# Optimization experiments

Measured on AMD Instinct MI355X. Metric: run time of the kernel, lower is better.

Reference implementation:

```python
import jax, jax.numpy as jnp
import numpy as np

N, E, IN, H1, H2, A, B, MAXB = 57344, 458752, 128, 256, 64, 11, 16, 4096
GD = H1  # g_dim = hidden1


def _lin(k, i, o):
    return jax.random.normal(k, (i, o), jnp.float32) / np.sqrt(i).astype(np.float32)


def setup_inputs():
    key = jax.random.key(0)
    ks = jax.random.split(key, 24)
    x = jax.random.normal(ks[0], (N, IN), jnp.float32)
    x = x.at[:, 0].set(1.0)  # every node is a host (x[:,0]==1)
    ei = jax.random.randint(ks[1], (2, E), 0, N, dtype=jnp.int32)
    sizes = [4096] * 12 + [2048] * 4  # sums to N
    batches = jnp.asarray(np.concatenate([[0], np.cumsum(sizes)]), jnp.int32)
    inp = {
        'x': x, 'ei': ei, 'batches': batches, 'max_batch': MAXB,
        'conv1_w': _lin(ks[2], IN, H1), 'conv1_b': jnp.zeros((H1,), jnp.float32),
        'conv2_w': _lin(ks[3], H1, H2), 'conv2_b': jnp.zeros((H2,), jnp.float32),
        # SimpleSelfAttention g0: in=IN, h=H1, g=GD
        'g0_aw': _lin(ks[4], IN, H1), 'g0_ab': jnp.zeros((H1,), jnp.float32),
        'g0_fw': _lin(ks[5], IN, H1), 'g0_fb': jnp.zeros((H1,), jnp.float32),
        'g0_gw': _lin(ks[6], H1 + GD, GD), 'g0_gb': jnp.zeros((GD,), jnp.float32),
        # g1: in=H1, h=H1, g=GD
        'g1_aw': _lin(ks[7], H1, H1), 'g1_ab': jnp.zeros((H1,), jnp.float32),
        'g1_fw': _lin(ks[8], H1, H1), 'g1_fb': jnp.zeros((H1,), jnp.float32),
        'g1_gw': _lin(ks[9], H1 + GD, GD), 'g1_gb': jnp.zeros((GD,), jnp.float32),
        # g2: in=H2, h=H2, g=GD
        'g2_aw': _lin(ks[10], H2, H2), 'g2_ab': jnp.zeros((H2,), jnp.float32),
        'g2_fw': _lin(ks[11], H2, H2), 'g2_fb': jnp.zeros((H2,), jnp.float32),
        'g2_gw': _lin(ks[12], H2 + GD, GD), 'g2_gb': jnp.zeros((GD,), jnp.float32),
        # out MLP head
        'o1_w': _lin(ks[13], H2 + GD, H1), 'o1_b': jnp.zeros((H1,), jnp.float32),
        'o2_w': _lin(ks[14], H1, A), 'o2_b': jnp.zeros((A,), jnp.float32),
    }
    return inp


def reference(x, ei, batches, max_batch,
              conv1_w, conv1_b, conv2_w, conv2_b,
              g0_aw, g0_ab, g0_fw, g0_fb, g0_gw, g0_gb,
              g1_aw, g1_ab, g1_fw, g1_fb, g1_gw, g1_gb,
              g2_aw, g2_ab, g2_fw, g2_fb, g2_gw, g2_gb,
              o1_w, o1_b, o2_w, o2_b):
    n = x.shape[0]
    nb = batches.shape[0] - 1
    idx = jnp.arange(n, dtype=jnp.int32)
    # all nodes are hosts; CSR -> (batch_id, position) for vectorized pad_and_pack
    batch_id = jnp.searchsorted(batches, idx, side='right').astype(jnp.int32) - 1
    pos = idx - batches[batch_id]
    mask = jnp.zeros((nb, max_batch, 1), x.dtype).at[batch_id, pos].set(1.0)

    def pack(h):  # [n, d] -> [nb, max_batch, d] with zero padding
        return jnp.zeros((nb, max_batch, h.shape[-1]), h.dtype).at[batch_id, pos].set(h)

    src_sl = jnp.concatenate([ei[0], idx])  # add self loops
    dst_sl = jnp.concatenate([ei[1], idx])

    def gcn(h, W, b):  # GCNConv: D^{-1/2}(A+I)D^{-1/2} h W + b (deg from target col)
        deg = jax.ops.segment_sum(jnp.ones_like(dst_sl, h.dtype), dst_sl, num_segments=n)
        dis = jnp.where(deg > 0, jax.lax.rsqrt(jnp.maximum(deg, 1.0)), 0.0)
        norm = dis[src_sl] * dis[dst_sl]
        hw = h @ W
        return jax.ops.segment_sum(hw[src_sl] * norm[:, None], dst_sl, num_segments=n) + b

    def attn(v, g, aw, ab, fw, fb, gw, gb):  # SimpleSelfAttention
        att = jax.nn.softmax(v @ aw + ab, axis=-1) * mask
        feat = v @ fw + fb
        o = jnp.sum(att * feat, axis=1)  # [nb, h]
        return g + (jnp.concatenate([o, g], axis=-1) @ gw + gb)

    g = attn(pack(x), jnp.zeros((nb, GD), x.dtype), g0_aw, g0_ab, g0_fw, g0_fb, g0_gw, g0_gb)
    h = jax.nn.relu(gcn(x, conv1_w, conv1_b))
    g = attn(pack(h), g, g1_aw, g1_ab, g1_fw, g1_fb, g1_gw, g1_gb)
    h = jax.nn.relu(gcn(h, conv2_w, conv2_b))
    g = attn(pack(h), g, g2_aw, g2_ab, g2_fw, g2_fb, g2_gw, g2_gb)

    host_z = jnp.concatenate([h, g[batch_id]], axis=1)  # repeat_interleave via gather
    actions = jax.nn.relu(host_z @ o1_w + o1_b) @ o2_w + o2_b  # [n, A]
    out = pack(actions)  # [nb, max_batch, A]
    out = jnp.where(mask > 0, out, -jnp.inf)
    return out.reshape(nb, max_batch * A)  # Categorical logits
```

## Files before the change

### kernel.cpp

```cpp
#include <hip/hip_runtime.h>
#include <math.h>

#define N_NODES 57344
#define N_EDGES 458752
#define DIM_IN 128
#define DIM_H1 256
#define DIM_H2 64
#define DIM_A 11
#define NB 16
#define MAXB 4096
#define OUT_PER_B (MAXB*DIM_A)
#define OUT_SZ (NB*OUT_PER_B)
#define NEG_FILL (-1.0e30f)

typedef unsigned short u16;
typedef unsigned int u32;
typedef __bf16 bf16x8 __attribute__((ext_vector_type(8)));
typedef float f32x4 __attribute__((ext_vector_type(4)));

__device__ __forceinline__ float bflo(u32 u){ union{u32 i; float f;} x; x.i = u<<16; return x.f; }
__device__ __forceinline__ float bfhi(u32 u){ union{u32 i; float f;} x; x.i = u & 0xFFFF0000u; return x.f; }
__device__ __forceinline__ u32 f2bf(float f){ union{float f; u32 i;} x; x.f=f; return (x.i + 0x7FFFu + ((x.i>>16)&1u)) >> 16; }

__device__ __forceinline__ float wave_max(float v){
  #pragma unroll
  for (int off=32; off; off>>=1) v = fmaxf(v, __shfl_xor(v, off));
  return v;
}
__device__ __forceinline__ float wave_sum(float v){
  #pragma unroll
  for (int off=32; off; off>>=1) v += __shfl_xor(v, off);
  return v;
}

__global__ __launch_bounds__(256) void k_init(int* cnt, int* bid, const int* __restrict__ batches,
                                              float* oacc, float* out){
  int i = blockIdx.x*256 + threadIdx.x;
  if (i < N_NODES){
    cnt[i] = 0;
    int lo=0, hi=NB-1;
    while (lo<hi){ int mid=(lo+hi+1)>>1; if (batches[mid]<=i) lo=mid; else hi=mid-1; }
    bid[i]=lo;
  }
  if (i < 3*NB*256) oacc[i] = 0.0f;
  if (i < OUT_SZ) out[i] = NEG_FILL;
}

__global__ __launch_bounds__(256) void k_deg(const int* __restrict__ ei, int* cnt){
  int e = blockIdx.x*256 + threadIdx.x;
  if (e < N_EDGES) atomicAdd(&cnt[ei[N_EDGES + e]], 1);
}

__global__ __launch_bounds__(256) void k_scanA(const int* __restrict__ cnt, int* bsum){
  __shared__ int s[256];
  int t=threadIdx.x; int i=blockIdx.x*256+t;
  s[t]=cnt[i]; __syncthreads();
  for (int off=128; off; off>>=1){ if (t<off) s[t]+=s[t+off]; __syncthreads(); }
  if (t==0) bsum[blockIdx.x]=s[0];
}
__global__ __launch_bounds__(256) void k_scanB(const int* __restrict__ bsum, int* boff){
  __shared__ int s[256];
  int t=threadIdx.x;
  int v = (t < N_NODES/256) ? bsum[t] : 0;
  s[t]=v; __syncthreads();
  for (int o=1;o<256;o<<=1){
    int a = (t>=o) ? s[t-o] : 0;
    __syncthreads();
    s[t] += a;
    __syncthreads();
  }
  if (t < N_NODES/256) boff[t] = s[t] - v;
}
__global__ __launch_bounds__(256) void k_scanC(const int* __restrict__ cnt, const int* __restrict__ boff,
                                               int* rowstart, int* cursor, float* dis){
  __shared__ int s[256];
  int t=threadIdx.x; int i=blockIdx.x*256+t;
  int v=cnt[i]; s[t]=v; __syncthreads();
  for (int off=1; off<256; off<<=1){
    int add = (t>=off)? s[t-off] : 0;
    __syncthreads();
    s[t]+=add;
    __syncthreads();
  }
  int rs = boff[blockIdx.x] + s[t] - v;
  rowstart[i]=rs; cursor[i]=rs;
  dis[i] = rsqrtf(1.0f + (float)v);
}
__global__ __launch_bounds__(256) void k_place(const int* __restrict__ ei, int* cursor, int* csr_src){
  int e = blockIdx.x*256 + threadIdx.x;
  if (e < N_EDGES){
    int s = ei[e], d = ei[N_EDGES+e];
    int slot = atomicAdd(&cursor[d], 1);
    csr_src[slot] = s;
  }
}

__global__ __launch_bounds__(256) void k_cvtx(const float* __restrict__ x, u16* __restrict__ xb){
  int i = blockIdx.x*256 + threadIdx.x;
  float4 v = *(const float4*)(x + (size_t)i*4);
  u32 lo = f2bf(v.x) | (f2bf(v.y)<<16);
  u32 hi = f2bf(v.z) | (f2bf(v.w)<<16);
  *(uint2*)(xb + (size_t)i*4) = make_uint2(lo, hi);
}

__global__ __launch_bounds__(256) void k_prep(
    const float* __restrict__ conv1_w, const float* __restrict__ g0_aw, const float* __restrict__ g0_fw,
    const float* __restrict__ g1_aw, const float* __restrict__ g1_fw, const float* __restrict__ conv2_w,
    const float* __restrict__ g2_aw, const float* __restrict__ g2_fw, const float* __restrict__ o1_w,
    const float* __restrict__ g0_ab, const float* __restrict__ g0_fb,
    const float* __restrict__ g1_ab, const float* __restrict__ g1_fb,
    const float* __restrict__ g2_ab, const float* __restrict__ g2_fb,
    u16* conv1T, u16* Wt0, u16* Wt1, u16* conv2T, u16* Wt2, u16* o1T,
    float* cb0, float* cb1, float* cb2){
  int i = blockIdx.x*256 + threadIdx.x;
  if (i < 32768){ int k=i>>8, n=i&255; conv1T[n*128+k]=(u16)f2bf(conv1_w[i]); return; } i-=32768;
  if (i < 32768){ int k=i>>8, n=i&255; Wt0[n*128+k]=(u16)f2bf(g0_aw[i]); return; } i-=32768;
  if (i < 32768){ int k=i>>8, n=i&255; Wt0[(256+n)*128+k]=(u16)f2bf(g0_fw[i]); return; } i-=32768;
  if (i < 65536){ int k=i>>8, n=i&255; Wt1[n*256+k]=(u16)f2bf(g1_aw[i]); return; } i-=65536;
  if (i < 65536){ int k=i>>8, n=i&255; Wt1[(256+n)*256+k]=(u16)f2bf(g1_fw[i]); return; } i-=65536;
  if (i < 16384){ int k=i>>6, n=i&63;  conv2T[n*256+k]=(u16)f2bf(conv2_w[i]); return; } i-=16384;
  if (i < 4096) { int k=i>>6, n=i&63;  Wt2[n*64+k]=(u16)f2bf(g2_aw[i]); return; } i-=4096;
  if (i < 4096) { int k=i>>6, n=i&63;  Wt2[(64+n)*64+k]=(u16)f2bf(g2_fw[i]); return; } i-=4096;
  if (i < 16384){ int k=i>>8, n=i&255; o1T[n*64+k]=(u16)f2bf(o1_w[i]); return; } i-=16384;
  if (i < 256){ cb0[i]=g0_ab[i]; return; } i-=256;
  if (i < 256){ cb0[256+i]=g0_fb[i]; return; } i-=256;
  if (i < 256){ cb1[i]=g1_ab[i]; return; } i-=256;
  if (i < 256){ cb1[256+i]=g1_fb[i]; return; } i-=256;
  if (i < 64) { cb2[i]=g2_ab[i]; return; } i-=64;
  if (i < 64) { cb2[64+i]=g2_fb[i]; return; }
}

__global__ __launch_bounds__(256) void k_agg1b(const u16* __restrict__ xb, const float* __restrict__ dis,
        const int* __restrict__ rowstart, const int* __restrict__ cnt, const int* __restrict__ csr_src,
        u16* __restrict__ agg){
  int d = (blockIdx.x*256 + threadIdx.x) >> 6;
  int lane = threadIdx.x & 63;
  float dd = dis[d];
  u32 u = *(const u32*)(xb + (size_t)d*DIM_IN + lane*2);
  float ax = bflo(u)*dd*dd, ay = bfhi(u)*dd*dd;
  int base = rowstart[d], c = cnt[d];
  int j = 0;
  for (; j+4 <= c; j += 4){
    int s0=csr_src[base+j+0], s1=csr_src[base+j+1], s2=csr_src[base+j+2], s3=csr_src[base+j+3];
    u32 u0=*(const u32*)(xb+(size_t)s0*DIM_IN+lane*2);
    u32 u1=*(const u32*)(xb+(size_t)s1*DIM_IN+lane*2);
    u32 u2=*(const u32*)(xb+(size_t)s2*DIM_IN+lane*2);
    u32 u3=*(const u32*)(xb+(size_t)s3*DIM_IN+lane*2);
    float n0=dis[s0]*dd, n1=dis[s1]*dd, n2=dis[s2]*dd, n3=dis[s3]*dd;
    ax=fmaf(bflo(u0),n0,ax); ay=fmaf(bfhi(u0),n0,ay);
    ax=fmaf(bflo(u1),n1,ax); ay=fmaf(bfhi(u1),n1,ay);
    ax=fmaf(bflo(u2),n2,ax); ay=fmaf(bfhi(u2),n2,ay);
    ax=fmaf(bflo(u3),n3,ax); ay=fmaf(bfhi(u3),n3,ay);
  }
  for (; j<c; ++j){
    int s = csr_src[base+j];
    float nrm = dis[s]*dd;
    u32 us = *(const u32*)(xb + (size_t)s*DIM_IN + lane*2);
    ax = fmaf(bflo(us), nrm, ax);
    ay = fmaf(bfhi(us), nrm, ay);
  }
  *(u32*)(agg + (size_t)d*DIM_IN + lane*2) = f2bf(ax) | (f2bf(ay)<<16);
}

__global__ __launch_bounds__(256) void k_agg2b(const u16* __restrict__ hw, const float* __restrict__ dis,
        const int* __restrict__ rowstart, const int* __restrict__ cnt, const int* __restrict__ csr_src,
        const float* __restrict__ b2, u16* __restrict__ h2){
  int d = (blockIdx.x*256 + threadIdx.x) >> 6;
  int lane = threadIdx.x & 63;
  float dd = dis[d];
  float acc = bflo((u32)hw[(size_t)d*DIM_H2 + lane]) * dd*dd;
  int base = rowstart[d], c = cnt[d];
  int j = 0;
  for (; j+4 <= c; j += 4){
    int s0=csr_src[base+j+0], s1=csr_src[base+j+1], s2=csr_src[base+j+2], s3=csr_src[base+j+3];
    u16 v0=hw[(size_t)s0*DIM_H2+lane], v1=hw[(size_t)s1*DIM_H2+lane];
    u16 v2=hw[(size_t)s2*DIM_H2+lane], v3=hw[(size_t)s3*DIM_H2+lane];
    float n0=dis[s0]*dd, n1=dis[s1]*dd, n2=dis[s2]*dd, n3=dis[s3]*dd;
    acc=fmaf(bflo((u32)v0),n0,acc); acc=fmaf(bflo((u32)v1),n1,acc);
    acc=fmaf(bflo((u32)v2),n2,acc); acc=fmaf(bflo((u32)v3),n3,acc);
  }
  for (; j<c; ++j){
    int s = csr_src[base+j];
    acc = fmaf(bflo((u32)hw[(size_t)s*DIM_H2 + lane]), dis[s]*dd, acc);
  }
  h2[(size_t)d*DIM_H2 + lane] = (u16)f2bf(fmaxf(acc + b2[lane], 0.0f));
}

__global__ __launch_bounds__(256) void k_mm(const u16* __restrict__ A, const u16* __restrict__ Wt,
        const float* __restrict__ bias, const float* __restrict__ rowbias, const int* __restrict__ bid,
        u16* __restrict__ C, int K, int Ncol, int flags){
  __shared__ u16 As[128][40];
  __shared__ u16 Bs[64][40];
  const int t = threadIdx.x;
  const int row0 = blockIdx.x*128, col0 = blockIdx.y*64;
  const int lane = t & 63, w = t >> 6;
  const int lr = lane & 15, q = lane >> 4;
  f32x4 acc[2][4];
  #pragma unroll
  for (int r=0;r<2;++r){
    #pragma unroll
    for (int c=0;c<4;++c){ f32x4 z = {}; acc[r][c] = z; }
  }
  for (int k0=0; k0<K; k0+=32){
    #pragma unroll
    for (int i=0;i<2;++i){
      int ch = t + i*256;
      int r = ch>>2, ko = (ch&3)*8;
      *(uint4*)(&As[r][ko]) = *(const uint4*)(A + (size_t)(row0+r)*K + k0 + ko);
    }
    {
      int r = t>>2, ko = (t&3)*8;
      *(uint4*)(&Bs[r][ko]) = *(const uint4*)(Wt + (size_t)(col0+r)*K + k0 + ko);
    }
    __syncthreads();
    bf16x8 af0 = *(const bf16x8*)(&As[w*32 + lr][q*8]);
    bf16x8 af1 = *(const bf16x8*)(&As[w*32 + 16 + lr][q*8]);
    #pragma unroll
    for (int c=0;c<4;++c){
      bf16x8 bfr = *(const bf16x8*)(&Bs[c*16 + lr][q*8]);
      acc[0][c] = __builtin_amdgcn_mfma_f32_16x16x32_bf16(af0, bfr, acc[0][c], 0,0,0);
      acc[1][c] = __builtin_amdgcn_mfma_f32_16x16x32_bf16(af1, bfr, acc[1][c], 0,0,0);
    }
    __syncthreads();
  }
  float bcol[4];
  #pragma unroll
  for (int c=0;c<4;++c){
    int col = col0 + c*16 + lr;
    float bv = 0.f;
    if (flags & 4) bv += bias[col];
    if (flags & 2) bv += rowbias[(size_t)bid[row0]*Ncol + col];
    bcol[c] = bv;
  }
  #pragma unroll
  for (int r=0;r<2;++r){
    #pragma unroll
    for (int c=0;c<4;++c){
      int col = col0 + c*16 + lr;
      #pragma unroll
      for (int i=0;i<4;++i){
        int row = row0 + w*32 + r*16 + q*4 + i;
        float v = acc[r][c][i] + bcol[c];
        if (flags & 1) v = fmaxf(v, 0.f);
        C[(size_t)row*Ncol + col] = (u16)f2bf(v);
      }
    }
  }
}

template<int DIN>
__global__ __launch_bounds__(256,2) void k_attn4(const u16* __restrict__ V, const u16* __restrict__ Wt,
        const float* __restrict__ cb, const int* __restrict__ bid, float* __restrict__ o){
  constexpr int KS  = DIN/32;
  constexpr int NJ  = 8*KS;
  constexpr int AST = DIN + 8;
  __shared__ u16 As[128*AST];
  __shared__ u16 Bs[2][64][40];
  const int t = threadIdx.x;
  const int node0 = blockIdx.x*128;
  const int lane = t & 63, w = t >> 6;
  const int lr = lane & 15, q = lane >> 4;
  #pragma unroll
  for (int i = 0; i < 128*DIN/(8*256); ++i){
    int ch = t + i*256;
    int r = ch / (DIN/8), co = (ch % (DIN/8))*8;
    *(uint4*)(&As[r*AST + co]) = *(const uint4*)(V + (size_t)(node0+r)*DIN + co);
  }
  auto stageB = [&](int j, int buf){
    int chunk = j / KS, k0 = j % KS;
    int r = t>>2, ko = (t&3)*8;
    *(uint4*)(&Bs[buf][r][ko]) = *(const uint4*)(Wt + (size_t)(chunk*64 + r)*DIN + k0*32 + ko);
  };
  f32x4 sacc[4][2][4];
  #pragma unroll
  for (int cc=0;cc<4;++cc)
    #pragma unroll
    for (int rf=0;rf<2;++rf)
      #pragma unroll
      for (int cf=0;cf<4;++cf){ f32x4 z = {}; sacc[cc][rf][cf] = z; }
  stageB(0, 0);
  __syncthreads();
  #pragma unroll
  for (int j=0; j<4*KS; ++j){
    if (j+1 < NJ) stageB(j+1, (j+1)&1);
    const int k0 = j % KS, chunk = j / KS, buf = j & 1;
    bf16x8 a0 = *(const bf16x8*)(&As[(w*32 + lr)*AST + k0*32 + q*8]);
    bf16x8 a1 = *(const bf16x8*)(&As[(w*32 + 16 + lr)*AST + k0*32 + q*8]);
    #pragma unroll
    for (int cf=0;cf<4;++cf){
      bf16x8 b = *(const bf16x8*)(&Bs[buf][cf*16 + lr][q*8]);
      sacc[chunk][0][cf] = __builtin_amdgcn_mfma_f32_16x16x32_bf16(a0, b, sacc[chunk][0][cf], 0,0,0);
      sacc[chunk][1][cf] = __builtin_amdgcn_mfma_f32_16x16x32_bf16(a1, b, sacc[chunk][1][cf], 0,0,0);
    }
    __syncthreads();
  }
  #pragma unroll
  for (int cc=0;cc<4;++cc)
    #pragma unroll
    for (int cf=0;cf<4;++cf){
      float bv = cb[cc*64 + cf*16 + lr];
      #pragma unroll
      for (int rf=0;rf<2;++rf)
        #pragma unroll
        for (int i=0;i<4;++i) sacc[cc][rf][cf][i] += bv;
    }
  float m[2][4], iz[2][4];
  #pragma unroll
  for (int rf=0;rf<2;++rf){
    #pragma unroll
    for (int i=0;i<4;++i){
      float mx = -1e30f;
      #pragma unroll
      for (int cc=0;cc<4;++cc)
        #pragma unroll
        for (int cf=0;cf<4;++cf) mx = fmaxf(mx, sacc[cc][rf][cf][i]);
      #pragma unroll
      for (int off=1; off<16; off<<=1) mx = fmaxf(mx, __shfl_xor(mx, off));
      float zz = 0.f;
      #pragma unroll
      for (int cc=0;cc<4;++cc)
        #pragma unroll
        for (int cf=0;cf<4;++cf) zz += __expf(sacc[cc][rf][cf][i] - mx);
      #pragma unroll
      for (int off=1; off<16; off<<=1) zz += __shfl_xor(zz, off);
      m[rf][i] = mx; iz[rf][i] = 1.0f/zz;
    }
  }
  const int bb = bid[node0];
  f32x4 facc[2][4];
  #pragma unroll
  for (int rf=0;rf<2;++rf)
    #pragma unroll
    for (int cf=0;cf<4;++cf){ f32x4 z = {}; facc[rf][cf] = z; }
  #pragma unroll
  for (int j=4*KS; j<NJ; ++j){
    if (j+1 < NJ) stageB(j+1, (j+1)&1);
    const int k0 = j % KS, chunk = j / KS, buf = j & 1;
    bf16x8 a0 = *(const bf16x8*)(&As[(w*32 + lr)*AST + k0*32 + q*8]);
    bf16x8 a1 = *(const bf16x8*)(&As[(w*32 + 16 + lr)*AST + k0*32 + q*8]);
    #pragma unroll
    for (int cf=0;cf<4;++cf){
      bf16x8 b = *(const bf16x8*)(&Bs[buf][cf*16 + lr][q*8]);
      facc[0][cf] = __builtin_amdgcn_mfma_f32_16x16x32_bf16(a0, b, facc[0][cf], 0,0,0);
      facc[1][cf] = __builtin_amdgcn_mfma_f32_16x16x32_bf16(a1, b, facc[1][cf], 0,0,0);
    }
    if (k0 == KS-1){
      const int sc = chunk - 4;
      #pragma unroll
      for (int cf=0;cf<4;++cf){
        float fb = cb[chunk*64 + cf*16 + lr];
        float cs = 0.f;
        #pragma unroll
        for (int rf=0;rf<2;++rf)
          #pragma unroll
          for (int i=0;i<4;++i){
            float p = __expf(sacc[sc][rf][cf][i] - m[rf][i]) * iz[rf][i];
            cs = fmaf(p, facc[rf][cf][i] + fb, cs);
          }
        cs += __shfl_xor(cs, 16);
        cs += __shfl_xor(cs, 32);
        if (q == 0) atomicAdd(&o[bb*256 + sc*64 + cf*16 + lr], cs);
      }
      #pragma unroll
      for (int rf=0;rf<2;++rf)
        #pragma unroll
        for (int cf=0;cf<4;++cf){ f32x4 z = {}; facc[rf][cf] = z; }
    }
    __syncthreads();
  }
}

template<int DIN, int H>
__global__ __launch_bounds__(256) void k_attnf(const u16* __restrict__ V, const u16* __restrict__ Wt,
        const float* __restrict__ cb, const int* __restrict__ bid, float* __restrict__ o){
  constexpr int CF  = H/64;
  constexpr int KS  = DIN/32;
  constexpr int AST = DIN + 8;
  constexpr int SST = H + 4;
  __shared__ u16 As[32*AST];
  __shared__ u16 Ssh[32*SST];
  __shared__ u16 Fsh[32*SST];
  __shared__ float mZ[2][32];
  const int t = threadIdx.x;
  const int node0 = blockIdx.x*32;
  const int lane = t & 63, w = t >> 6;
  const int lr = lane & 15, q = lane >> 4;
  #pragma unroll
  for (int i = 0; i < (32*DIN/8)/256; ++i){
    int ch = t + i*256;
    int r = ch / (DIN/8), co = (ch % (DIN/8))*8;
    *(uint4*)(&As[r*AST + co]) = *(const uint4*)(V + (size_t)(node0+r)*DIN + co);
  }
  __syncthreads();
  #pragma unroll
  for (int ph = 0; ph < 2; ++ph){
    f32x4 acc[2][CF];
    #pragma unroll
    for (int r=0;r<2;++r){
      #pragma unroll
      for (int c=0;c<CF;++c){ f32x4 z = {}; acc[r][c] = z; }
    }
    #pragma unroll
    for (int k=0;k<KS;++k){
      bf16x8 a0 = *(const bf16x8*)(&As[lr*AST + k*32 + q*8]);
      bf16x8 a1 = *(const bf16x8*)(&As[(16+lr)*AST + k*32 + q*8]);
      #pragma unroll
      for (int c=0;c<CF;++c){
        int col = ph*H + w*(16*CF) + c*16 + lr;
        bf16x8 b = *(const bf16x8*)(Wt + (size_t)col*DIN + k*32 + q*8);
        acc[0][c] = __builtin_amdgcn_mfma_f32_16x16x32_bf16(a0, b, acc[0][c], 0,0,0);
        acc[1][c] = __builtin_amdgcn_mfma_f32_16x16x32_bf16(a1, b, acc[1][c], 0,0,0);
      }
    }
    u16* dst = ph ? Fsh : Ssh;
    #pragma unroll
    for (int c=0;c<CF;++c){
      int colL = w*(16*CF) + c*16 + lr;
      float bias = cb[ph*H + colL];
      #pragma unroll
      for (int rf=0; rf<2; ++rf){
        #pragma unroll
        for (int i=0;i<4;++i){
          int row = rf*16 + q*4 + i;
          dst[row*SST + colL] = (u16)f2bf(acc[rf][c][i] + bias);
        }
      }
    }
    if (ph==0){
      __syncthreads();
      #pragma unroll
      for (int nn=0; nn<8; ++nn){
        int n = w*8 + nn;
        constexpr int VPL = H/64;
        float vals[VPL]; float mx = -1e30f;
        if constexpr (VPL == 4){
          uint2 uv = *(const uint2*)(&Ssh[n*SST + lane*4]);
          vals[0]=bflo(uv.x); vals[1]=bfhi(uv.x); vals[2]=bflo(uv.y); vals[3]=bfhi(uv.y);
          mx = fmaxf(fmaxf(vals[0],vals[1]), fmaxf(vals[2],vals[3]));
        } else {
          vals[0] = bflo((u32)Ssh[n*SST + lane]);
          mx = vals[0];
        }
        mx = wave_max(mx);
        float z = 0.f;
        #pragma unroll
        for (int i=0;i<VPL;++i) z += __expf(vals[i]-mx);
        z = wave_sum(z);
        if (lane==0){ mZ[0][n]=mx; mZ[1][n]=1.0f/z; }
      }
    }
  }
  __syncthreads();
  const int col = t % H;
  constexpr int NPER = 32*H/256;
  const int n0 = (t / H) * NPER;
  float acc2 = 0.f;
  #pragma unroll 8
  for (int n=n0; n<n0+NPER; ++n){
    float s = bflo((u32)Ssh[n*SST + col]);
    float f = bflo((u32)Fsh[n*SST + col]);
    acc2 = fmaf(__expf(s - mZ[0][n]) * mZ[1][n], f, acc2);
  }
  atomicAdd(&o[bid[node0]*H + col], acc2);
}

template<int H, bool HASG>
__global__ __launch_bounds__(256) void k_gup2(const float* __restrict__ o, const float* __restrict__ gprev,
        const float* __restrict__ gw, const float* __restrict__ gb, float* __restrict__ gout){
  constexpr int KT = H + (HASG ? 256 : 0);
  constexpr int KPS = KT/8;
  __shared__ float vsh[KT];
  __shared__ float red[8][33];
  const int b = blockIdx.x;
  const int c = threadIdx.x & 31;
  const int s = threadIdx.x >> 5;
  const int col = blockIdx.y*32 + c;
  for (int k=threadIdx.x; k<KT; k+=256)
    vsh[k] = (k < H) ? o[b*H + k] : gprev[b*256 + (k - H)];
  __syncthreads();
  float acc = 0.f;
  const float* wp = gw + (size_t)(s*KPS)*256 + col;
  #pragma unroll 8
  for (int i=0;i<KPS;++i)
    acc = fmaf(vsh[s*KPS+i], wp[(size_t)i*256], acc);
  red[s][c] = acc;
  __syncthreads();
  if (s==0){
    float sum = 0.f;
    #pragma unroll
    for (int j=0;j<8;++j) sum += red[j][c];
    float gp = HASG ? gprev[b*256+col] : 0.f;
    gout[b*256+col] = gp + sum + gb[col];
  }
}

__global__ __launch_bounds__(256) void k_hb2(const float* __restrict__ g2, const float* __restrict__ o1w,
                                             const float* __restrict__ o1b, float* __restrict__ hb){
  __shared__ float vsh[256];
  __shared__ float red[8][33];
  const int b = blockIdx.x;
  const int c = threadIdx.x & 31;
  const int s = threadIdx.x >> 5;
  const int col = blockIdx.y*32 + c;
  vsh[threadIdx.x] = g2[b*256 + threadIdx.x];
  __syncthreads();
  float acc = 0.f;
  const float* wp = o1w + (size_t)(64 + s*32)*256 + col;
  #pragma unroll 8
  for (int i=0;i<32;++i)
    acc = fmaf(vsh[s*32+i], wp[(size_t)i*256], acc);
  red[s][c] = acc;
  __syncthreads();
  if (s==0){
    float sum = 0.f;
    #pragma unroll
    for (int j=0;j<8;++j) sum += red[j][c];
    hb[b*256+col] = sum + o1b[col];
  }
}

__global__ __launch_bounds__(256) void k_head2(const u16* __restrict__ z, const float* __restrict__ w,
        const float* __restrict__ bvec, const int* __restrict__ bid, const int* __restrict__ batches,
        float* __restrict__ out){
  __shared__ float zs[16][257];
  int t = threadIdx.x;
  int g0 = blockIdx.x*16;
  #pragma unroll
  for (int i=0;i<2;++i){
    int ch = t + i*256;
    int v = ch>>5, ko=(ch&31)*8;
    uint4 qv = *(const uint4*)(z + (size_t)(g0+v)*256 + ko);
    zs[v][ko+0]=bflo(qv.x); zs[v][ko+1]=bfhi(qv.x);
    zs[v][ko+2]=bflo(qv.y); zs[v][ko+3]=bfhi(qv.y);
    zs[v][ko+4]=bflo(qv.z); zs[v][ko+5]=bfhi(qv.z);
    zs[v][ko+6]=bflo(qv.w); zs[v][ko+7]=bfhi(qv.w);
  }
  __syncthreads();
  int v = t >> 4, c = t & 15;
  if (c < DIM_A){
    float acc = bvec[c];
    for (int k=0;k<256;++k) acc = fmaf(zs[v][k], w[k*DIM_A + c], acc);
    int node = g0 + v;
    int bb = bid[node];
    out[(size_t)bb*OUT_PER_B + (size_t)(node - batches[bb])*DIM_A + c] = acc;
  }
}

extern "C" void kernel_launch(void* const* d_in, const int* in_sizes, int n_in,
                              void* d_out, int out_size, void* d_ws, size_t ws_size,
                              hipStream_t stream){
  const float* x       = (const float*)d_in[0];
  const int*   ei      = (const int*)d_in[1];
  const int*   batches = (const int*)d_in[2];
  const float* conv1_w = (const float*)d_in[4];
  const float* conv1_b = (const float*)d_in[5];
  const float* conv2_w = (const float*)d_in[6];
  const float* conv2_b = (const float*)d_in[7];
  const float* g0_aw = (const float*)d_in[8];  const float* g0_ab = (const float*)d_in[9];
  const float* g0_fw = (const float*)d_in[10]; const float* g0_fb = (const float*)d_in[11];
  const float* g0_gw = (const float*)d_in[12]; const float* g0_gb = (const float*)d_in[13];
  const float* g1_aw = (const float*)d_in[14]; const float* g1_ab = (const float*)d_in[15];
  const float* g1_fw = (const float*)d_in[16]; const float* g1_fb = (const float*)d_in[17];
  const float* g1_gw = (const float*)d_in[18]; const float* g1_gb = (const float*)d_in[19];
  const float* g2_aw = (const float*)d_in[20]; const float* g2_ab = (const float*)d_in[21];
  const float* g2_fw = (const float*)d_in[22]; const float* g2_fb = (const float*)d_in[23];
  const float* g2_gw = (const float*)d_in[24]; const float* g2_gb = (const float*)d_in[25];
  const float* o1_w  = (const float*)d_in[26]; const float* o1_b  = (const float*)d_in[27];
  const float* o2_w  = (const float*)d_in[28]; const float* o2_b  = (const float*)d_in[29];
  float* out = (float*)d_out;

  char* W = (char*)d_ws;
  size_t off = 0;
  auto alloc = [&](size_t bytes)->void*{
    off = (off + 255) & ~(size_t)255;
    void* p = W + off; off += bytes; return p;
  };
  float* dis      = (float*)alloc(N_NODES*4);
  int*   cnt      = (int*)  alloc(N_NODES*4);
  int*   bid      = (int*)  alloc(N_NODES*4);
  int*   rowstart = (int*)  alloc(N_NODES*4);
  int*   cursor   = (int*)  alloc(N_NODES*4);
  int*   csr_src  = (int*)  alloc(N_EDGES*4);
  int*   bsum     = (int*)  alloc(256*4);
  int*   boff     = (int*)  alloc(256*4);
  float* o0       = (float*)alloc(NB*256*4);
  float* o1a      = (float*)alloc(NB*256*4);
  float* o2a      = (float*)alloc(NB*256*4);
  float* gv0      = (float*)alloc(NB*256*4);
  float* gv1      = (float*)alloc(NB*256*4);
  float* gv2      = (float*)alloc(NB*256*4);
  float* hb       = (float*)alloc(NB*256*4);
  float* cb0      = (float*)alloc(512*4);
  float* cb1      = (float*)alloc(512*4);
  float* cb2      = (float*)alloc(128*4);
  u16* conv1T = (u16*)alloc(32768*2);
  u16* Wt0    = (u16*)alloc(65536*2);
  u16* Wt1    = (u16*)alloc(131072*2);
  u16* conv2T = (u16*)alloc(16384*2);
  u16* Wt2    = (u16*)alloc(8192*2);
  u16* o1T    = (u16*)alloc(16384*2);
  u16* h1b    = (u16*)alloc((size_t)N_NODES*DIM_H1*2);
  u16* X      = (u16*)alloc((size_t)N_NODES*DIM_IN*2);
  u16* agg1b  = (u16*)alloc((size_t)N_NODES*DIM_IN*2);
  u16* xb    = X;
  u16* hw2b  = X;
  u16* h2b   = X + (size_t)N_NODES*DIM_H2;
  u16* z     = h1b;

  k_init <<<OUT_SZ/256, 256, 0, stream>>>(cnt, bid, batches, o0, out);
  k_deg  <<<N_EDGES/256, 256, 0, stream>>>(ei, cnt);
  k_scanA<<<N_NODES/256, 256, 0, stream>>>(cnt, bsum);
  k_scanB<<<1, 256, 0, stream>>>(bsum, boff);
  k_scanC<<<N_NODES/256, 256, 0, stream>>>(cnt, boff, rowstart, cursor, dis);
  k_place<<<N_EDGES/256, 256, 0, stream>>>(ei, cursor, csr_src);

  k_cvtx <<<N_NODES*DIM_IN/4/256, 256, 0, stream>>>(x, xb);
  k_prep <<<(270336+1152+255)/256, 256, 0, stream>>>(conv1_w, g0_aw, g0_fw, g1_aw, g1_fw, conv2_w,
            g2_aw, g2_fw, o1_w, g0_ab, g0_fb, g1_ab, g1_fb, g2_ab, g2_fb,
            conv1T, Wt0, Wt1, conv2T, Wt2, o1T, cb0, cb1, cb2);

  k_agg1b<<<N_NODES/4, 256, 0, stream>>>(xb, dis, rowstart, cnt, csr_src, agg1b);
  k_mm   <<<dim3(N_NODES/128, 4), 256, 0, stream>>>(agg1b, conv1T, conv1_b, nullptr, nullptr,
                                                    h1b, DIM_IN, DIM_H1, 4|1);
  k_attn4<128><<<N_NODES/128, 256, 0, stream>>>(xb, Wt0, cb0, bid, o0);
  k_gup2<256,false><<<dim3(NB,8), 256, 0, stream>>>(o0, nullptr, g0_gw, g0_gb, gv0);

  k_attn4<256><<<N_NODES/128, 256, 0, stream>>>(h1b, Wt1, cb1, bid, o1a);
  k_gup2<256,true><<<dim3(NB,8), 256, 0, stream>>>(o1a, gv0, g1_gw, g1_gb, gv1);

  k_mm   <<<dim3(N_NODES/128, 1), 256, 0, stream>>>(h1b, conv2T, nullptr, nullptr, nullptr,
                                                    hw2b, DIM_H1, DIM_H2, 0);
  k_agg2b<<<N_NODES/4, 256, 0, stream>>>(hw2b, dis, rowstart, cnt, csr_src, conv2_b, h2b);

  k_attnf<64,64><<<N_NODES/32, 256, 0, stream>>>(h2b, Wt2, cb2, bid, o2a);
  k_gup2<64,true><<<dim3(NB,8), 256, 0, stream>>>(o2a, gv1, g2_gw, g2_gb, gv2);

  k_hb2  <<<dim3(NB,8), 256, 0, stream>>>(gv2, o1_w, o1_b, hb);
  k_mm   <<<dim3(N_NODES/128, 4), 256, 0, stream>>>(h2b, o1T, nullptr, hb, bid, z, DIM_H2, 256, 2|1);
  k_head2<<<N_NODES/16, 256, 0, stream>>>(z, o2_w, o2_b, bid, batches, out);

  (void)in_sizes; (void)n_in; (void)out_size; (void)ws_size;
}
```

Before: 423.3 us.

## Add split-wave fused attention kernel for layer-1 self-attention pooling

Replaces the layer-1 attention kernel with a new variant that processes 64 nodes per block. Two waves compute the softmax logits and two compute the feature projection from a shared LDS tile of V. Softmax row max and sum are reduced across the two score waves via shared memory, and probabilities are staged through LDS as bf16 for the feature waves, which then atomically add per-batch sums. This is meant to cut the recomputation and serial loop of the older kernel, at the cost of large accumulator register use, more blocks and more atomics, and bf16 rounding of the probabilities.

```diff
diff --git a/kernel.cpp b/kernel.cpp
--- a/kernel.cpp
+++ b/kernel.cpp
@@ -367,6 +367,121 @@
         for (int cf=0;cf<4;++cf){ f32x4 z = {}; facc[rf][cf] = z; }
     }
     __syncthreads();
+  }
+}
+
+template<int DIN>
+__global__ __launch_bounds__(256,2) void k_attnU2(const u16* __restrict__ V, const u16* __restrict__ Wt,
+        const float* __restrict__ cb, const int* __restrict__ bid, float* __restrict__ o){
+  constexpr int KS  = DIN/32;
+  constexpr int AST = DIN + 8;
+  constexpr int PST = 256 + 8;
+  __shared__ u16 As[64*AST];
+  __shared__ float mred[2][64];
+  __shared__ float zred[2][64];
+  const int t = threadIdx.x;
+  const int node0 = blockIdx.x*64;
+  const int lane = t & 63, w = t >> 6;
+  const int lr = lane & 15, q = lane >> 4;
+  const int bb = bid[node0];
+  #pragma unroll
+  for (int i = 0; i < 64*DIN/(8*256); ++i){
+    int ch = t + i*256;
+    int r = ch / (DIN/8), co = (ch % (DIN/8))*8;
+    *(uint4*)(&As[r*AST + co]) = *(const uint4*)(V + (size_t)(node0+r)*DIN + co);
+  }
+  __syncthreads();
+  f32x4 acc[4][8];
+  #pragma unroll
+  for (int rf=0;rf<4;++rf)
+    #pragma unroll
+    for (int cf=0;cf<8;++cf){ f32x4 z = {}; acc[rf][cf] = z; }
+  const u16* Wb = Wt + (size_t)(w*128 + lr)*DIN + q*8;
+  #pragma unroll
+  for (int k0=0;k0<KS;++k0){
+    bf16x8 b[8];
+    #pragma unroll
+    for (int cf=0;cf<8;++cf)
+      b[cf] = *(const bf16x8*)(Wb + (size_t)(cf*16)*DIN + k0*32);
+    bf16x8 a[4];
+    #pragma unroll
+    for (int rf=0;rf<4;++rf) a[rf] = *(const bf16x8*)(&As[(rf*16+lr)*AST + k0*32 + q*8]);
+    #pragma unroll
+    for (int cf=0;cf<8;++cf)
+      #pragma unroll
+      for (int rf=0;rf<4;++rf)
+        acc[rf][cf] = __builtin_amdgcn_mfma_f32_16x16x32_bf16(a[rf], b[cf], acc[rf][cf], 0,0,0);
+  }
+  #pragma unroll
+  for (int cf=0;cf<8;++cf){
+    float bv = cb[w*128 + cf*16 + lr];
+    #pragma unroll
+    for (int rf=0;rf<4;++rf)
+      #pragma unroll
+      for (int i=0;i<4;++i) acc[rf][cf][i] += bv;
+  }
+  u16* Psh = As;
+  const bool isS = (w < 2);
+  if (isS){
+    #pragma unroll
+    for (int rf=0;rf<4;++rf)
+      #pragma unroll
+      for (int i=0;i<4;++i){
+        float pm = acc[rf][0][i];
+        #pragma unroll
+        for (int cf=1;cf<8;++cf) pm = fmaxf(pm, acc[rf][cf][i]);
+        #pragma unroll
+        for (int off=1; off<16; off<<=1) pm = fmaxf(pm, __shfl_xor(pm, off));
+        if (lr==0) mred[w][rf*16 + q*4 + i] = pm;
+      }
+  }
+  __syncthreads();
+  if (isS){
+    #pragma unroll
+    for (int rf=0;rf<4;++rf)
+      #pragma unroll
+      for (int i=0;i<4;++i){
+        int row = rf*16 + q*4 + i;
+        float m = fmaxf(mred[0][row], mred[1][row]);
+        float pz = 0.f;
+        #pragma unroll
+        for (int cf=0;cf<8;++cf) pz += __expf(acc[rf][cf][i] - m);
+        #pragma unroll
+        for (int off=1; off<16; off<<=1) pz += __shfl_xor(pz, off);
+        if (lr==0) zred[w][row] = pz;
+      }
+  }
+  __syncthreads();
+  if (isS){
+    #pragma unroll
+    for (int rf=0;rf<4;++rf)
+      #pragma unroll
+      for (int i=0;i<4;++i){
+        int row = rf*16 + q*4 + i;
+        float m  = fmaxf(mred[0][row], mred[1][row]);
+        float iz = 1.0f/(zred[0][row] + zred[1][row]);
+        #pragma unroll
+        for (int cf=0;cf<8;++cf)
+          Psh[row*PST + w*128 + cf*16 + lr] = (u16)f2bf(__expf(acc[rf][cf][i]-m)*iz);
+      }
+  }
+  __syncthreads();
+  if (!isS){
+    #pragma unroll
+    for (int cf=0;cf<8;++cf){
+      const int pcol = (w-2)*128 + cf*16 + lr;
+      float cs = 0.f;
+      #pragma unroll
+      for (int rf=0;rf<4;++rf)
+        #pragma unroll
+        for (int i=0;i<4;++i){
+          float p = bflo((u32)Psh[(rf*16 + q*4 + i)*PST + pcol]);
+          cs = fmaf(p, acc[rf][cf][i], cs);
+        }
+      cs += __shfl_xor(cs, 16);
+      cs += __shfl_xor(cs, 32);
+      if (q == 0) atomicAdd(&o[bb*256 + pcol], cs);
+    }
   }
 }
 
@@ -625,7 +740,7 @@
   k_attn4<128><<<N_NODES/128, 256, 0, stream>>>(xb, Wt0, cb0, bid, o0);
   k_gup2<256,false><<<dim3(NB,8), 256, 0, stream>>>(o0, nullptr, g0_gw, g0_gb, gv0);
 
-  k_attn4<256><<<N_NODES/128, 256, 0, stream>>>(h1b, Wt1, cb1, bid, o1a);
+  k_attnU2<256><<<N_NODES/64, 256, 0, stream>>>(h1b, Wt1, cb1, bid, o1a);
   k_gup2<256,true><<<dim3(NB,8), 256, 0, stream>>>(o1a, gv0, g1_gw, g1_gb, gv1);
 
   k_mm   <<<dim3(N_NODES/128, 1), 256, 0, stream>>>(h1b, conv2T, nullptr, nullptr, nullptr,
```

Measured after the change: 433.9 us. 2.5% more time.
